# Optimization experiments

Hardware: AMD Instinct MI355X
Metric: run time of the kernel (lower is better)

## Reference

```python
import jax, jax.numpy as jnp
import numpy as np
import math

S, B, H, NH = 2048, 2, 2048, 16
HD = H // NH
COEFF = 1.0  # layer_number = 1
NORM = math.sqrt(HD) * COEFF
MASK_VAL = -10000.0


def setup_inputs() -> dict:
    key = jax.random.key(0)
    ks = jax.random.split(key, 4)
    hidden_states = jax.random.normal(ks[0], (S, B, H), dtype=jnp.float32)
    # causal mask: True = masked (Megatron convention)
    attention_mask = jnp.triu(jnp.ones((S, S), dtype=bool), k=1)[None, None]
    w_qkv = jax.random.normal(ks[1], (H, 3 * H), dtype=jnp.float32) * (1.0 / math.sqrt(H))
    b_qkv = jnp.zeros((3 * H,), dtype=jnp.float32)
    w_dense = jax.random.normal(ks[2], (H, H), dtype=jnp.float32) * (1.0 / math.sqrt(H))
    b_dense = jnp.zeros((H,), dtype=jnp.float32)
    return {"hidden_states": hidden_states, "attention_mask": attention_mask,
            "w_qkv": w_qkv, "b_qkv": b_qkv, "w_dense": w_dense, "b_dense": b_dense}


def reference(hidden_states, attention_mask, w_qkv, b_qkv, w_dense, b_dense):
    s, b, h = hidden_states.shape
    # QKV projection: [s, b, 3h] -> [s, b, nh, 3*hd] -> split
    mixed = hidden_states @ w_qkv + b_qkv
    mixed = mixed.reshape(s, b, NH, 3 * HD)
    q, k, v = jnp.split(mixed, 3, axis=-1)  # each [s, b, nh, hd]
    # raw scores scaled by 1/(sqrt(hd)*coeff)  -> [b, nh, s_q, s_k]
    scores = jnp.einsum('sbnd,tbnd->bnst', q, k) / NORM
    # fused scale-mask-softmax in fp32 with scale=coeff (net 1/sqrt(hd))
    scores32 = scores.astype(jnp.float32) * COEFF
    scores32 = jnp.where(attention_mask, MASK_VAL, scores32)
    probs = jax.nn.softmax(scores32, axis=-1).astype(hidden_states.dtype)
    # dropout p=0.0 -> identity
    context = jnp.einsum('bnst,tbnd->sbnd', probs, v).reshape(s, b, h)
    # row-parallel dense with skip_bias_add: bias returned separately
    output = context @ w_dense
    return output, b_dense
```

## Files before the change

kernel.cpp:

```cpp
#include <hip/hip_runtime.h>
#include <hip/hip_bf16.h>

constexpr int S   = 2048;
constexpr int B   = 2;
constexpr int H   = 2048;
constexpr int NH  = 16;
constexpr int HD  = 128;
constexpr int K3H = 3 * H;
constexpr float SCALE2 = 0.08838834764831845f * 1.4426950408889634f;
constexpr float MSHIFT = 12.0f;

typedef __attribute__((ext_vector_type(8))) short short8;
typedef __attribute__((ext_vector_type(4))) float f32x4;

__device__ __forceinline__ ushort f2b(float f) {
  uint u = __float_as_uint(f);
  return (ushort)((u + 0x7fffu + ((u >> 16) & 1u)) >> 16);
}

__device__ __forceinline__ f32x4 mfma16(short8 a, short8 b, f32x4 c) {
  return __builtin_amdgcn_mfma_f32_16x16x32_bf16(a, b, c, 0, 0, 0);
}

__device__ __forceinline__ void gld16(const ushort* g, ushort* l) {
  __builtin_amdgcn_global_load_lds((const __attribute__((address_space(1))) void*)g,
                                   (__attribute__((address_space(3))) void*)l,
                                   16, 0, 0);
}

__global__ __launch_bounds__(256) void cast_bf16(const float* __restrict__ src,
                                                 ushort* __restrict__ dst, int n) {
  int i = (blockIdx.x * 256 + threadIdx.x) * 4;
  if (i >= n) return;
  float4 v = *(const float4*)(src + i);
  ushort4 o;
  o.x = f2b(v.x); o.y = f2b(v.y); o.z = f2b(v.z); o.w = f2b(v.w);
  *(ushort4*)(dst + i) = o;
}

__global__ __launch_bounds__(256) void transpose_cast(const float* __restrict__ src,
                                                      ushort* __restrict__ dst,
                                                      int R, int C) {
  __shared__ ushort tile[32][33];
  int c0 = blockIdx.x * 32, r0 = blockIdx.y * 32;
  int tx = threadIdx.x, ty = threadIdx.y;
#pragma unroll
  for (int i = 0; i < 4; i++) {
    int r = r0 + ty + i * 8;
    tile[ty + i * 8][tx] = f2b(src[(size_t)r * C + c0 + tx]);
  }
  __syncthreads();
#pragma unroll
  for (int i = 0; i < 4; i++) {
    int c = c0 + ty + i * 8;
    dst[(size_t)c * R + r0 + tx] = tile[tx][ty + i * 8];
  }
}

template <int MODE>
__global__ __launch_bounds__(256) void gemm_bt(const ushort* __restrict__ A,
                                               const ushort* __restrict__ Bt,
                                               const float* __restrict__ bias,
                                               void* __restrict__ out0,
                                               void* __restrict__ out1,
                                               int M, int N, int K) {
  __shared__ ushort lds_a[128 * 64];
  __shared__ ushort lds_b[128 * 64];
  const int tid  = threadIdx.x;
  const int wave = tid >> 6, lane = tid & 63;
  const int quad = lane >> 4, l15 = lane & 15;
  const int wr = wave >> 1, wc = wave & 1;
  const int m0 = blockIdx.y * 128, n0 = blockIdx.x * 128;

  f32x4 acc[4][4] = {};

  const int srow   = tid >> 3;
  const int schunk = (tid & 7) ^ (srow & 7);
  const ushort* gaS = A  + (size_t)(m0 + srow) * K + schunk * 8;
  const ushort* gbS = Bt + (size_t)(n0 + srow) * K + schunk * 8;

  const int fsw = l15 & 7;

  const int nk = K >> 6;
  for (int kt = 0; kt < nk; kt++) {
    const int ko = kt * 64;
#pragma unroll
    for (int j = 0; j < 4; j++) {
      gld16(gaS + (size_t)(j * 32) * K + ko, &lds_a[(j * 256 + wave * 64) * 8]);
      gld16(gbS + (size_t)(j * 32) * K + ko, &lds_b[(j * 256 + wave * 64) * 8]);
    }
    __syncthreads();

#pragma unroll
    for (int ks = 0; ks < 2; ks++) {
      short8 af[4], bq[4];
#pragma unroll
      for (int mt = 0; mt < 4; mt++)
        af[mt] = *(const short8*)&lds_a[((wr * 64 + mt * 16 + l15) * 8 + ((ks * 4 + quad) ^ fsw)) * 8];
#pragma unroll
      for (int nt = 0; nt < 4; nt++)
        bq[nt] = *(const short8*)&lds_b[((wc * 64 + nt * 16 + l15) * 8 + ((ks * 4 + quad) ^ fsw)) * 8];
#pragma unroll
      for (int mt = 0; mt < 4; mt++)
#pragma unroll
        for (int nt = 0; nt < 4; nt++)
          acc[mt][nt] = mfma16(af[mt], bq[nt], acc[mt][nt]);
    }
    __syncthreads();
  }

  if (MODE == 1) {
#pragma unroll
    for (int nt = 0; nt < 4; nt++) {
      const int col = n0 + wc * 64 + nt * 16 + l15;
      const int nh  = col / 384;
      const int rem = col - nh * 384;
      const float bv = bias[col];
      if (rem < 256) {
        ushort* qk = (ushort*)out0;
#pragma unroll
        for (int mt = 0; mt < 4; mt++) {
          const int rb = m0 + wr * 64 + mt * 16 + quad * 4;
#pragma unroll
          for (int i = 0; i < 4; i++)
            qk[((size_t)(rb + i) * NH + nh) * 256 + rem] = f2b(acc[mt][nt][i] + bv);
        }
      } else {
        ushort* vt = (ushort*)out1;
        const size_t colbase = ((size_t)nh * 128 + (rem - 256)) * S;
#pragma unroll
        for (int mt = 0; mt < 4; mt++) {
          const int rb = m0 + wr * 64 + mt * 16 + quad * 4;
#pragma unroll
          for (int i = 0; i < 4; i++) {
            const int row = rb + i;
            vt[(size_t)(row & 1) * ((size_t)NH * 128 * S) + colbase + (row >> 1)]
                = f2b(acc[mt][nt][i] + bv);
          }
        }
      }
    }
  } else {
    float* Co = (float*)out0;
#pragma unroll
    for (int mt = 0; mt < 4; mt++)
#pragma unroll
      for (int nt = 0; nt < 4; nt++) {
        const int col = n0 + wc * 64 + nt * 16 + l15;
#pragma unroll
        for (int i = 0; i < 4; i++) {
          const int row = m0 + wr * 64 + mt * 16 + quad * 4 + i;
          Co[(size_t)row * N + col] = acc[mt][nt][i];
        }
      }
  }
}

__global__ __launch_bounds__(512) void flash_attn(const ushort* __restrict__ qkb,
                                                  const ushort* __restrict__ VtG,
                                                  ushort* __restrict__ ctxb) {
  __shared__ ushort Ks[2][64 * 128];
  __shared__ ushort Vt[2][128 * 64];
  __shared__ ushort Pls[8][16 * 64];

  const int tid  = threadIdx.x;
  const int wave = tid >> 6, lane = tid & 63;
  const int quad = lane >> 4, l15 = lane & 15;
  const int jj = blockIdx.x;
  const int nh = blockIdx.y, b = blockIdx.z;
  const int stA = jj, stB = 15 - jj;
  const int nA = 2 * jj + 2;
  constexpr int TOT = 34;

  ushort* Pw = Pls[wave];

  const int ktRow = tid >> 4;
  const int kCol  = (tid & 15) ^ (ktRow & 15);
  const ushort* kS = qkb + (((size_t)(ktRow * B + b) * NH + nh) * 256 + 128 + kCol * 8);
  const int vdRow = tid >> 3;
  const int vCol  = (tid & 7) ^ (vdRow & 7);
  const ushort* vS = VtG + ((size_t)(b * NH + nh) * 128 + vdRow) * (size_t)S + vCol * 8;

  const size_t kRowStep32 = (size_t)32 * B * NH * 256;
  const size_t vRowStep64 = (size_t)64 * S;
  const size_t kTileStep  = (size_t)64 * B * NH * 256;

  auto stageTile = [&](int kt, int nxt) {
    const size_t ko = (size_t)kt * kTileStep;
    const int vo = kt * 64;
    gld16(kS + ko, &Ks[nxt][(wave * 64) * 8]);
    gld16(kS + ko + kRowStep32, &Ks[nxt][(512 + wave * 64) * 8]);
    gld16(vS + vo, &Vt[nxt][(wave * 64) * 8]);
    gld16(vS + vo + vRowStep64, &Vt[nxt][(512 + wave * 64) * 8]);
  };

  short8 qf[4];
  int q0 = stA * 128;
  {
    const ushort* qPtr = qkb + (((size_t)((q0 + wave * 16 + l15) * B + b) * NH + nh) * 256 + quad * 8);
#pragma unroll
    for (int ks = 0; ks < 4; ks++) qf[ks] = *(const short8*)(qPtr + ks * 32);
  }

  float l_r[4];
  f32x4 acc_o[8];
#pragma unroll
  for (int i = 0; i < 4; i++) l_r[i] = 0.0f;
#pragma unroll
  for (int j = 0; j < 8; j++) acc_o[j] = (f32x4){0.f, 0.f, 0.f, 0.f};

  stageTile(0, 0);
  __syncthreads();

  for (int it = 0; it < TOT; it++) {
    const int buf = it & 1;
    const int kt = (it < nA) ? it : it - nA;
    const int t0 = kt * 64;

    if (it + 1 < TOT)
      stageTile((it + 1 < nA) ? it + 1 : it + 1 - nA, buf ^ 1);

    f32x4 sa[4];
#pragma unroll
    for (int nt = 0; nt < 4; nt++) sa[nt] = (f32x4){0.f, 0.f, 0.f, 0.f};
#pragma unroll
    for (int ks = 0; ks < 4; ks++) {
#pragma unroll
      for (int nt = 0; nt < 4; nt++) {
        const int gs = (ks * 4 + quad) ^ l15;
        short8 bq = *(const short8*)&Ks[buf][((nt * 16 + l15) * 16 + gs) * 8];
        sa[nt] = mfma16(qf[ks], bq, sa[nt]);
      }
    }

    const int qw0 = q0 + wave * 16;
    const bool diag = (t0 + 63 > qw0);
#pragma unroll
    for (int i = 0; i < 4; i++) {
      const int qg = qw0 + quad * 4 + i;
      const int prow = quad * 4 + i;
      float lacc = l_r[i];
#pragma unroll
      for (int nt = 0; nt < 4; nt++) {
        float e = fmaf(sa[nt][i], SCALE2, -MSHIFT);
        if (diag) {
          const int tg = t0 + nt * 16 + l15;
          if (tg > qg) e = -1e30f;
        }
        const float p = exp2f(e);
        lacc += p;
        const int gs = (nt * 2 + (l15 >> 3)) ^ (prow & 7);
        Pw[prow * 64 + gs * 8 + (l15 & 7)] = f2b(p);
      }
      l_r[i] = lacc;
    }

#pragma unroll
    for (int ks2 = 0; ks2 < 2; ks2++) {
      const int pg = (ks2 * 4 + quad) ^ (l15 & 7);
      short8 a2 = *(const short8*)&Pw[l15 * 64 + pg * 8];
#pragma unroll
      for (int j = 0; j < 8; j++) {
        const int gs = (ks2 * 4 + quad) ^ (l15 & 7);
        short8 b2 = *(const short8*)&Vt[buf][((j * 16 + l15) * 8 + gs) * 8];
        acc_o[j] = mfma16(a2, b2, acc_o[j]);
      }
    }

    if (it == nA - 1) {
#pragma unroll
      for (int i = 0; i < 4; i++) {
        float ls = l_r[i];
#pragma unroll
        for (int off = 1; off < 16; off <<= 1) ls += __shfl_xor(ls, off);
        const float inv = 1.0f / ls;
        const int qg = q0 + wave * 16 + quad * 4 + i;
        ushort* dst = ctxb + ((size_t)qg * B + b) * H + nh * HD;
#pragma unroll
        for (int j = 0; j < 8; j++)
          dst[j * 16 + l15] = f2b(acc_o[j][i] * inv);
      }
      q0 = stB * 128;
      const ushort* qPtr = qkb + (((size_t)((q0 + wave * 16 + l15) * B + b) * NH + nh) * 256 + quad * 8);
#pragma unroll
      for (int ks = 0; ks < 4; ks++) qf[ks] = *(const short8*)(qPtr + ks * 32);
#pragma unroll
      for (int i = 0; i < 4; i++) l_r[i] = 0.0f;
#pragma unroll
      for (int j = 0; j < 8; j++) acc_o[j] = (f32x4){0.f, 0.f, 0.f, 0.f};
    }

    __syncthreads();
  }

#pragma unroll
  for (int i = 0; i < 4; i++) {
    float ls = l_r[i];
#pragma unroll
    for (int off = 1; off < 16; off <<= 1) ls += __shfl_xor(ls, off);
    const float inv = 1.0f / ls;
    const int qg = q0 + wave * 16 + quad * 4 + i;
    ushort* dst = ctxb + ((size_t)qg * B + b) * H + nh * HD;
#pragma unroll
    for (int j = 0; j < 8; j++)
      dst[j * 16 + l15] = f2b(acc_o[j][i] * inv);
  }
}

extern "C" void kernel_launch(void* const* d_in, const int* in_sizes, int n_in,
                              void* d_out, int out_size, void* d_ws, size_t ws_size,
                              hipStream_t stream) {
  (void)in_sizes; (void)n_in; (void)out_size; (void)ws_size;
  const float* hs     = (const float*)d_in[0];
  const float* wqkv   = (const float*)d_in[2];
  const float* bqkv   = (const float*)d_in[3];
  const float* wdense = (const float*)d_in[4];
  const float* bdense = (const float*)d_in[5];
  float* out = (float*)d_out;

  ushort* Xb      = (ushort*)d_ws;
  ushort* WqkvT   = Xb      + (size_t)S * B * H;
  ushort* WdenseT = WqkvT   + (size_t)H * K3H;
  ushort* qkb     = WdenseT + (size_t)H * H;
  ushort* VtG     = qkb     + (size_t)S * B * NH * 256;
  ushort* ctxb    = VtG     + (size_t)B * NH * HD * S;

  cast_bf16<<<dim3((S * B * H) / 1024), dim3(256), 0, stream>>>(hs, Xb, S * B * H);
  transpose_cast<<<dim3(K3H / 32, H / 32), dim3(32, 8), 0, stream>>>(wqkv, WqkvT, H, K3H);
  transpose_cast<<<dim3(H / 32, H / 32), dim3(32, 8), 0, stream>>>(wdense, WdenseT, H, H);

  gemm_bt<1><<<dim3(K3H / 128, (S * B) / 128), dim3(256), 0, stream>>>(
      Xb, WqkvT, bqkv, qkb, VtG, S * B, K3H, H);

  flash_attn<<<dim3(8, NH, B), dim3(512), 0, stream>>>(qkb, VtG, ctxb);

  gemm_bt<0><<<dim3(H / 128, (S * B) / 128), dim3(256), 0, stream>>>(
      ctxb, WdenseT, nullptr, out, nullptr, S * B, H, H);

  hipMemcpyAsync(out + (size_t)S * B * H, bdense, H * sizeof(float),
                 hipMemcpyDeviceToDevice, stream);
}
```

Before: 404.9 us.

## Triple-buffer GEMM LDS with 256x128 tiles and 8-wave blocks

Rewrites the bf16 GEMM main loop to use a three-stage LDS ring buffer. Global loads for tile kt+2 are issued while MFMAs run on tile kt, with manual vmcnt waits and barriers in place of full __syncthreads. The block tile grows to 256x128 with 512 threads, and s_setprio is raised around the MFMA burst. This targets global-load latency stalls, at the cost of much larger LDS use (about 144KB per block) and fewer blocks per CU.

```diff
diff --git a/kernel.cpp b/kernel.cpp
--- a/kernel.cpp
+++ b/kernel.cpp
@@ -58,19 +58,19 @@
 }
 
 template <int MODE>
-__global__ __launch_bounds__(256) void gemm_bt(const ushort* __restrict__ A,
-                                               const ushort* __restrict__ Bt,
-                                               const float* __restrict__ bias,
-                                               void* __restrict__ out0,
-                                               void* __restrict__ out1,
-                                               int M, int N, int K) {
-  __shared__ ushort lds_a[128 * 64];
-  __shared__ ushort lds_b[128 * 64];
+__global__ __launch_bounds__(512, 2) void gemm_bt(const ushort* __restrict__ A,
+                                                  const ushort* __restrict__ Bt,
+                                                  const float* __restrict__ bias,
+                                                  void* __restrict__ out0,
+                                                  void* __restrict__ out1,
+                                                  int M, int N, int K) {
+  __shared__ __align__(16) ushort lds_a[3][256 * 64];
+  __shared__ __align__(16) ushort lds_b[3][128 * 64];
   const int tid  = threadIdx.x;
   const int wave = tid >> 6, lane = tid & 63;
   const int quad = lane >> 4, l15 = lane & 15;
-  const int wr = wave >> 1, wc = wave & 1;
-  const int m0 = blockIdx.y * 128, n0 = blockIdx.x * 128;
+  const int wm = wave >> 1, wn = wave & 1;
+  const int m0 = blockIdx.y * 256, n0 = blockIdx.x * 128;
 
   f32x4 acc[4][4] = {};
 
@@ -78,41 +78,64 @@
   const int schunk = (tid & 7) ^ (srow & 7);
   const ushort* gaS = A  + (size_t)(m0 + srow) * K + schunk * 8;
   const ushort* gbS = Bt + (size_t)(n0 + srow) * K + schunk * 8;
+  const size_t rs64 = (size_t)64 * K;
 
   const int fsw = l15 & 7;
 
-  const int nk = K >> 6;
-  for (int kt = 0; kt < nk; kt++) {
-    const int ko = kt * 64;
-#pragma unroll
-    for (int j = 0; j < 4; j++) {
-      gld16(gaS + (size_t)(j * 32) * K + ko, &lds_a[(j * 256 + wave * 64) * 8]);
-      gld16(gbS + (size_t)(j * 32) * K + ko, &lds_b[(j * 256 + wave * 64) * 8]);
-    }
-    __syncthreads();
-
-#pragma unroll
-    for (int ks = 0; ks < 2; ks++) {
-      short8 af[4], bq[4];
+  auto stageH = [&](int kt, int bf, int h) {
+    const size_t ko = (size_t)kt * 64;
+    gld16(gaS + (size_t)(2 * h)     * rs64 + ko, &lds_a[bf][((2 * h)     * 512 + wave * 64) * 8]);
+    gld16(gaS + (size_t)(2 * h + 1) * rs64 + ko, &lds_a[bf][((2 * h + 1) * 512 + wave * 64) * 8]);
+    gld16(gbS + (size_t)h           * rs64 + ko, &lds_b[bf][(h * 512 + wave * 64) * 8]);
+  };
+
+  const int NT = K >> 6;
+
+  stageH(0, 0, 0); stageH(0, 0, 1);
+  stageH(1, 1, 0); stageH(1, 1, 1);
+  asm volatile("s_waitcnt vmcnt(6)" ::: "memory");
+  __builtin_amdgcn_s_barrier();
+
+  int bf = 0;
+  for (int kt = 0; kt < NT; ++kt) {
+    const bool pf = (kt + 2 < NT);
+    const int nf = (kt + 2) % 3;
+    short8 af[4], bq[4];
+
+#pragma unroll
+    for (int kk = 0; kk < 2; ++kk) {
 #pragma unroll
       for (int mt = 0; mt < 4; mt++)
-        af[mt] = *(const short8*)&lds_a[((wr * 64 + mt * 16 + l15) * 8 + ((ks * 4 + quad) ^ fsw)) * 8];
+        af[mt] = *(const short8*)&lds_a[bf][((wm * 64 + mt * 16 + l15) * 8 + ((kk * 4 + quad) ^ fsw)) * 8];
 #pragma unroll
       for (int nt = 0; nt < 4; nt++)
-        bq[nt] = *(const short8*)&lds_b[((wc * 64 + nt * 16 + l15) * 8 + ((ks * 4 + quad) ^ fsw)) * 8];
+        bq[nt] = *(const short8*)&lds_b[bf][((wn * 64 + nt * 16 + l15) * 8 + ((kk * 4 + quad) ^ fsw)) * 8];
+      if (pf) stageH(kt + 2, nf, kk);
+      __builtin_amdgcn_s_barrier();
+      asm volatile("s_waitcnt lgkmcnt(0)" ::: "memory");
+      __builtin_amdgcn_sched_barrier(0);
+      __builtin_amdgcn_s_setprio(1);
 #pragma unroll
       for (int mt = 0; mt < 4; mt++)
 #pragma unroll
         for (int nt = 0; nt < 4; nt++)
           acc[mt][nt] = mfma16(af[mt], bq[nt], acc[mt][nt]);
-    }
-    __syncthreads();
+      __builtin_amdgcn_s_setprio(0);
+      if (kk == 0) __builtin_amdgcn_s_barrier();
+    }
+
+    if (kt + 1 < NT) {
+      if (pf) asm volatile("s_waitcnt vmcnt(6)" ::: "memory");
+      else    asm volatile("s_waitcnt vmcnt(0)" ::: "memory");
+      __builtin_amdgcn_s_barrier();
+    }
+    bf = (bf + 1 == 3) ? 0 : bf + 1;
   }
 
   if (MODE == 1) {
 #pragma unroll
     for (int nt = 0; nt < 4; nt++) {
-      const int col = n0 + wc * 64 + nt * 16 + l15;
+      const int col = n0 + wn * 64 + nt * 16 + l15;
       const int nh  = col / 384;
       const int rem = col - nh * 384;
       const float bv = bias[col];
@@ -120,7 +143,7 @@
         ushort* qk = (ushort*)out0;
 #pragma unroll
         for (int mt = 0; mt < 4; mt++) {
-          const int rb = m0 + wr * 64 + mt * 16 + quad * 4;
+          const int rb = m0 + wm * 64 + mt * 16 + quad * 4;
 #pragma unroll
           for (int i = 0; i < 4; i++)
             qk[((size_t)(rb + i) * NH + nh) * 256 + rem] = f2b(acc[mt][nt][i] + bv);
@@ -130,7 +153,7 @@
         const size_t colbase = ((size_t)nh * 128 + (rem - 256)) * S;
 #pragma unroll
         for (int mt = 0; mt < 4; mt++) {
-          const int rb = m0 + wr * 64 + mt * 16 + quad * 4;
+          const int rb = m0 + wm * 64 + mt * 16 + quad * 4;
 #pragma unroll
           for (int i = 0; i < 4; i++) {
             const int row = rb + i;
@@ -146,10 +169,10 @@
     for (int mt = 0; mt < 4; mt++)
 #pragma unroll
       for (int nt = 0; nt < 4; nt++) {
-        const int col = n0 + wc * 64 + nt * 16 + l15;
+        const int col = n0 + wn * 64 + nt * 16 + l15;
 #pragma unroll
         for (int i = 0; i < 4; i++) {
-          const int row = m0 + wr * 64 + mt * 16 + quad * 4 + i;
+          const int row = m0 + wm * 64 + mt * 16 + quad * 4 + i;
           Co[(size_t)row * N + col] = acc[mt][nt][i];
         }
       }
@@ -329,12 +352,12 @@
   transpose_cast<<<dim3(K3H / 32, H / 32), dim3(32, 8), 0, stream>>>(wqkv, WqkvT, H, K3H);
   transpose_cast<<<dim3(H / 32, H / 32), dim3(32, 8), 0, stream>>>(wdense, WdenseT, H, H);
 
-  gemm_bt<1><<<dim3(K3H / 128, (S * B) / 128), dim3(256), 0, stream>>>(
+  gemm_bt<1><<<dim3(K3H / 128, (S * B) / 256), dim3(512), 0, stream>>>(
       Xb, WqkvT, bqkv, qkb, VtG, S * B, K3H, H);
 
   flash_attn<<<dim3(8, NH, B), dim3(512), 0, stream>>>(qkb, VtG, ctxb);
 
-  gemm_bt<0><<<dim3(H / 128, (S * B) / 128), dim3(256), 0, stream>>>(
+  gemm_bt<0><<<dim3(H / 128, (S * B) / 256), dim3(512), 0, stream>>>(
       ctxb, WdenseT, nullptr, out, nullptr, S * B, H, H);
 
   hipMemcpyAsync(out + (size_t)S * B * H, bdense, H * sizeof(float),
```

Result: no change. 402.0 us (-0.7%).

## Double-buffer GEMM LDS tiles and split attention into smaller 64-row blocks

Applied to the files above, without the earlier changes.

The GEMM now double-buffers its A/B LDS tiles, prefetching the next k-tile while computing the current one, and uses one barrier per iteration instead of two. Flash attention switches from 512-thread blocks covering 128-row query tiles to 256-thread blocks covering 64-row tiles, paired to balance causal work, which doubles the grid to 512 blocks. s_setprio is also raised around the MFMA sections. The GEMM's shared memory doubles, which may limit occupancy, and the attention change trades fewer waves per block for more blocks.

```diff
diff --git a/kernel.cpp b/kernel.cpp
--- a/kernel.cpp
+++ b/kernel.cpp
@@ -58,14 +58,14 @@
 }
 
 template <int MODE>
-__global__ __launch_bounds__(256) void gemm_bt(const ushort* __restrict__ A,
-                                               const ushort* __restrict__ Bt,
-                                               const float* __restrict__ bias,
-                                               void* __restrict__ out0,
-                                               void* __restrict__ out1,
-                                               int M, int N, int K) {
-  __shared__ ushort lds_a[128 * 64];
-  __shared__ ushort lds_b[128 * 64];
+__global__ __launch_bounds__(256, 2) void gemm_bt(const ushort* __restrict__ A,
+                                                  const ushort* __restrict__ Bt,
+                                                  const float* __restrict__ bias,
+                                                  void* __restrict__ out0,
+                                                  void* __restrict__ out1,
+                                                  int M, int N, int K) {
+  __shared__ __align__(16) ushort lds_a[2][128 * 64];
+  __shared__ __align__(16) ushort lds_b[2][128 * 64];
   const int tid  = threadIdx.x;
   const int wave = tid >> 6, lane = tid & 63;
   const int quad = lane >> 4, l15 = lane & 15;
@@ -81,32 +81,49 @@
 
   const int fsw = l15 & 7;
 
-  const int nk = K >> 6;
-  for (int kt = 0; kt < nk; kt++) {
-    const int ko = kt * 64;
+  auto stageT = [&](int kt, int bf) {
+    const size_t ko = (size_t)kt * 64;
 #pragma unroll
     for (int j = 0; j < 4; j++) {
-      gld16(gaS + (size_t)(j * 32) * K + ko, &lds_a[(j * 256 + wave * 64) * 8]);
-      gld16(gbS + (size_t)(j * 32) * K + ko, &lds_b[(j * 256 + wave * 64) * 8]);
-    }
-    __syncthreads();
-
-#pragma unroll
-    for (int ks = 0; ks < 2; ks++) {
-      short8 af[4], bq[4];
+      gld16(gaS + (size_t)(j * 32) * K + ko, &lds_a[bf][(j * 256 + wave * 64) * 8]);
+      gld16(gbS + (size_t)(j * 32) * K + ko, &lds_b[bf][(j * 256 + wave * 64) * 8]);
+    }
+  };
+
+  const int NT = K >> 6;
+
+  stageT(0, 0);
+  asm volatile("s_waitcnt vmcnt(0)" ::: "memory");
+  __builtin_amdgcn_s_barrier();
+
+  for (int kt = 0; kt < NT; ++kt) {
+    const int bf = kt & 1;
+
+    if (kt + 1 < NT) stageT(kt + 1, bf ^ 1);
+
+    short8 af[2][4], bq[2][4];
+#pragma unroll
+    for (int kk = 0; kk < 2; ++kk) {
 #pragma unroll
       for (int mt = 0; mt < 4; mt++)
-        af[mt] = *(const short8*)&lds_a[((wr * 64 + mt * 16 + l15) * 8 + ((ks * 4 + quad) ^ fsw)) * 8];
+        af[kk][mt] = *(const short8*)&lds_a[bf][((wr * 64 + mt * 16 + l15) * 8 + ((kk * 4 + quad) ^ fsw)) * 8];
 #pragma unroll
       for (int nt = 0; nt < 4; nt++)
-        bq[nt] = *(const short8*)&lds_b[((wc * 64 + nt * 16 + l15) * 8 + ((ks * 4 + quad) ^ fsw)) * 8];
+        bq[kk][nt] = *(const short8*)&lds_b[bf][((wc * 64 + nt * 16 + l15) * 8 + ((kk * 4 + quad) ^ fsw)) * 8];
+    }
+
+#pragma unroll
+    for (int kk = 0; kk < 2; ++kk)
 #pragma unroll
       for (int mt = 0; mt < 4; mt++)
 #pragma unroll
         for (int nt = 0; nt < 4; nt++)
-          acc[mt][nt] = mfma16(af[mt], bq[nt], acc[mt][nt]);
-    }
-    __syncthreads();
+          acc[mt][nt] = mfma16(af[kk][mt], bq[kk][nt], acc[mt][nt]);
+
+    if (kt + 1 < NT) {
+      asm volatile("s_waitcnt vmcnt(0)" ::: "memory");
+      __builtin_amdgcn_s_barrier();
+    }
   }
 
   if (MODE == 1) {
@@ -156,21 +173,21 @@
   }
 }
 
-__global__ __launch_bounds__(512) void flash_attn(const ushort* __restrict__ qkb,
+__global__ __launch_bounds__(256) void flash_attn(const ushort* __restrict__ qkb,
                                                   const ushort* __restrict__ VtG,
                                                   ushort* __restrict__ ctxb) {
   __shared__ ushort Ks[2][64 * 128];
   __shared__ ushort Vt[2][128 * 64];
-  __shared__ ushort Pls[8][16 * 64];
+  __shared__ ushort Pls[4][16 * 64];
 
   const int tid  = threadIdx.x;
   const int wave = tid >> 6, lane = tid & 63;
   const int quad = lane >> 4, l15 = lane & 15;
   const int jj = blockIdx.x;
   const int nh = blockIdx.y, b = blockIdx.z;
-  const int stA = jj, stB = 15 - jj;
-  const int nA = 2 * jj + 2;
-  constexpr int TOT = 34;
+  const int stA = jj, stB = 31 - jj;
+  const int nA = jj + 1;
+  constexpr int TOT = 33;
 
   ushort* Pw = Pls[wave];
 
@@ -181,21 +198,23 @@
   const int vCol  = (tid & 7) ^ (vdRow & 7);
   const ushort* vS = VtG + ((size_t)(b * NH + nh) * 128 + vdRow) * (size_t)S + vCol * 8;
 
-  const size_t kRowStep32 = (size_t)32 * B * NH * 256;
-  const size_t vRowStep64 = (size_t)64 * S;
+  const size_t kRowStep16 = (size_t)16 * B * NH * 256;
+  const size_t vRowStep32 = (size_t)32 * S;
   const size_t kTileStep  = (size_t)64 * B * NH * 256;
 
   auto stageTile = [&](int kt, int nxt) {
     const size_t ko = (size_t)kt * kTileStep;
     const int vo = kt * 64;
-    gld16(kS + ko, &Ks[nxt][(wave * 64) * 8]);
-    gld16(kS + ko + kRowStep32, &Ks[nxt][(512 + wave * 64) * 8]);
-    gld16(vS + vo, &Vt[nxt][(wave * 64) * 8]);
-    gld16(vS + vo + vRowStep64, &Vt[nxt][(512 + wave * 64) * 8]);
+#pragma unroll
+    for (int c = 0; c < 4; c++)
+      gld16(kS + ko + c * kRowStep16, &Ks[nxt][(c * 256 + wave * 64) * 8]);
+#pragma unroll
+    for (int c = 0; c < 4; c++)
+      gld16(vS + vo + c * vRowStep32, &Vt[nxt][(c * 256 + wave * 64) * 8]);
   };
 
   short8 qf[4];
-  int q0 = stA * 128;
+  int q0 = stA * 64;
   {
     const ushort* qPtr = qkb + (((size_t)((q0 + wave * 16 + l15) * B + b) * NH + nh) * 256 + quad * 8);
 #pragma unroll
@@ -223,6 +242,7 @@
     f32x4 sa[4];
 #pragma unroll
     for (int nt = 0; nt < 4; nt++) sa[nt] = (f32x4){0.f, 0.f, 0.f, 0.f};
+    __builtin_amdgcn_s_setprio(1);
 #pragma unroll
     for (int ks = 0; ks < 4; ks++) {
 #pragma unroll
@@ -232,6 +252,7 @@
         sa[nt] = mfma16(qf[ks], bq, sa[nt]);
       }
     }
+    __builtin_amdgcn_s_setprio(0);
 
     const int qw0 = q0 + wave * 16;
     const bool diag = (t0 + 63 > qw0);
@@ -255,6 +276,7 @@
       l_r[i] = lacc;
     }
 
+    __builtin_amdgcn_s_setprio(1);
 #pragma unroll
     for (int ks2 = 0; ks2 < 2; ks2++) {
       const int pg = (ks2 * 4 + quad) ^ (l15 & 7);
@@ -266,6 +288,7 @@
         acc_o[j] = mfma16(a2, b2, acc_o[j]);
       }
     }
+    __builtin_amdgcn_s_setprio(0);
 
     if (it == nA - 1) {
 #pragma unroll
@@ -280,7 +303,7 @@
         for (int j = 0; j < 8; j++)
           dst[j * 16 + l15] = f2b(acc_o[j][i] * inv);
       }
-      q0 = stB * 128;
+      q0 = stB * 64;
       const ushort* qPtr = qkb + (((size_t)((q0 + wave * 16 + l15) * B + b) * NH + nh) * 256 + quad * 8);
 #pragma unroll
       for (int ks = 0; ks < 4; ks++) qf[ks] = *(const short8*)(qPtr + ks * 32);
@@ -332,7 +355,7 @@
   gemm_bt<1><<<dim3(K3H / 128, (S * B) / 128), dim3(256), 0, stream>>>(
       Xb, WqkvT, bqkv, qkb, VtG, S * B, K3H, H);
 
-  flash_attn<<<dim3(8, NH, B), dim3(512), 0, stream>>>(qkb, VtG, ctxb);
+  flash_attn<<<dim3(16, NH, B), dim3(256), 0, stream>>>(qkb, VtG, ctxb);
 
   gemm_bt<0><<<dim3(H / 128, (S * B) / 128), dim3(256), 0, stream>>>(
       ctxb, WdenseT, nullptr, out, nullptr, S * B, H, H);
```

After: 399.8 us. No clear change (-1.3%).

## Triple-buffer GEMM LDS tiles with async prefetch two K-steps ahead

Applied to the files above, without the earlier changes.

Rewrites the bf16 GEMM main loop from a single 64-wide K tile with two barriers per iteration to a three-stage ring of 32-wide K tiles. Global-to-LDS loads for step kt+2 are issued before the MFMAs of step kt, with explicit vmcnt waits and one barrier per step. The aim is to hide global memory latency behind compute. In exchange it does more loop iterations, changes the LDS swizzle to a 4-chunk pattern, and adds an occupancy hint of 3 blocks per CU.

```diff
diff --git a/kernel.cpp b/kernel.cpp
--- a/kernel.cpp
+++ b/kernel.cpp
@@ -58,14 +58,14 @@
 }
 
 template <int MODE>
-__global__ __launch_bounds__(256) void gemm_bt(const ushort* __restrict__ A,
-                                               const ushort* __restrict__ Bt,
-                                               const float* __restrict__ bias,
-                                               void* __restrict__ out0,
-                                               void* __restrict__ out1,
-                                               int M, int N, int K) {
-  __shared__ ushort lds_a[128 * 64];
-  __shared__ ushort lds_b[128 * 64];
+__global__ __launch_bounds__(256, 3) void gemm_bt(const ushort* __restrict__ A,
+                                                  const ushort* __restrict__ Bt,
+                                                  const float* __restrict__ bias,
+                                                  void* __restrict__ out0,
+                                                  void* __restrict__ out1,
+                                                  int M, int N, int K) {
+  __shared__ __align__(16) ushort lds_a[3][128 * 32];
+  __shared__ __align__(16) ushort lds_b[3][128 * 32];
   const int tid  = threadIdx.x;
   const int wave = tid >> 6, lane = tid & 63;
   const int quad = lane >> 4, l15 = lane & 15;
@@ -74,39 +74,57 @@
 
   f32x4 acc[4][4] = {};
 
-  const int srow   = tid >> 3;
-  const int schunk = (tid & 7) ^ (srow & 7);
+  const int srow   = tid >> 2;
+  const int schunk = (tid & 3) ^ (srow & 3);
   const ushort* gaS = A  + (size_t)(m0 + srow) * K + schunk * 8;
   const ushort* gbS = Bt + (size_t)(n0 + srow) * K + schunk * 8;
-
-  const int fsw = l15 & 7;
-
-  const int nk = K >> 6;
-  for (int kt = 0; kt < nk; kt++) {
-    const int ko = kt * 64;
-#pragma unroll
-    for (int j = 0; j < 4; j++) {
-      gld16(gaS + (size_t)(j * 32) * K + ko, &lds_a[(j * 256 + wave * 64) * 8]);
-      gld16(gbS + (size_t)(j * 32) * K + ko, &lds_b[(j * 256 + wave * 64) * 8]);
-    }
-    __syncthreads();
-
-#pragma unroll
-    for (int ks = 0; ks < 2; ks++) {
-      short8 af[4], bq[4];
-#pragma unroll
-      for (int mt = 0; mt < 4; mt++)
-        af[mt] = *(const short8*)&lds_a[((wr * 64 + mt * 16 + l15) * 8 + ((ks * 4 + quad) ^ fsw)) * 8];
+  const size_t rs64 = (size_t)64 * K;
+
+  const int fsw = l15 & 3;
+
+  auto stageT = [&](int kt, int bf) {
+    const size_t ko = (size_t)kt * 32;
+#pragma unroll
+    for (int j = 0; j < 2; j++) {
+      gld16(gaS + (size_t)j * rs64 + ko, &lds_a[bf][(j * 256 + wave * 64) * 8]);
+      gld16(gbS + (size_t)j * rs64 + ko, &lds_b[bf][(j * 256 + wave * 64) * 8]);
+    }
+  };
+
+  const int NT = K >> 5;
+
+  stageT(0, 0);
+  stageT(1, 1);
+  asm volatile("s_waitcnt vmcnt(4)" ::: "memory");
+  __builtin_amdgcn_s_barrier();
+
+  int bf = 0;
+  for (int kt = 0; kt < NT; ++kt) {
+    short8 af[4], bq[4];
+#pragma unroll
+    for (int mt = 0; mt < 4; mt++)
+      af[mt] = *(const short8*)&lds_a[bf][((wr * 64 + mt * 16 + l15) * 4 + (quad ^ fsw)) * 8];
+#pragma unroll
+    for (int nt = 0; nt < 4; nt++)
+      bq[nt] = *(const short8*)&lds_b[bf][((wc * 64 + nt * 16 + l15) * 4 + (quad ^ fsw)) * 8];
+
+    if (kt + 2 < NT) {
+      const int nf = (bf + 2 >= 3) ? bf - 1 : bf + 2;
+      stageT(kt + 2, nf);
+    }
+
+#pragma unroll
+    for (int mt = 0; mt < 4; mt++)
 #pragma unroll
       for (int nt = 0; nt < 4; nt++)
-        bq[nt] = *(const short8*)&lds_b[((wc * 64 + nt * 16 + l15) * 8 + ((ks * 4 + quad) ^ fsw)) * 8];
-#pragma unroll
-      for (int mt = 0; mt < 4; mt++)
-#pragma unroll
-        for (int nt = 0; nt < 4; nt++)
-          acc[mt][nt] = mfma16(af[mt], bq[nt], acc[mt][nt]);
-    }
-    __syncthreads();
+        acc[mt][nt] = mfma16(af[mt], bq[nt], acc[mt][nt]);
+
+    if (kt + 1 < NT) {
+      if (kt + 2 < NT) asm volatile("s_waitcnt vmcnt(4)" ::: "memory");
+      else             asm volatile("s_waitcnt vmcnt(0)" ::: "memory");
+      __builtin_amdgcn_s_barrier();
+    }
+    bf = (bf + 1 == 3) ? 0 : bf + 1;
   }
 
   if (MODE == 1) {
```

After: 404.7 us. About the same (-0.0%).
